# Optimization experiments

Measured on AMD Instinct MI355X. Metric: run time of the kernel, lower is better.

The kernel has to match this reference:

```python
import jax
import jax.numpy as jnp
from jax import lax
import numpy as np

L, B, D_IN, D = 1024, 16, 2048, 2048
K = 3  # n_in == n_out -> k = 3, highway uses x directly


def setup_inputs() -> dict:
    key = jax.random.key(0)
    k1, k2 = jax.random.split(key)
    x = jax.random.normal(k1, (L, B, D_IN), dtype=jnp.float32)
    c0 = jnp.zeros((B, D), dtype=jnp.float32)
    # learned params: projection weight (n_in, n_out*k) and bias (2*n_out)
    weight = jax.random.normal(k2, (D_IN, D * K), dtype=jnp.float32) * (1.0 / np.sqrt(D_IN))
    bias = jnp.zeros((2 * D,), dtype=jnp.float32)
    return {"x": x, "c0": c0, "weight": weight, "bias": bias}


def reference(x, c0, weight, bias):
    # x: [L, B, n_in], c0: [B, d], weight: [n_in, d*3], bias: [2*d]
    Llen, Bsz, _ = x.shape
    d = c0.shape[-1]
    u = jnp.einsum("lbi,ik->lbk", x, weight).reshape(Llen, Bsz, d, K)
    u0 = u[..., 0]                                   # candidate
    g1 = jax.nn.sigmoid(u[..., 1] + bias[:d])        # forget gate
    g2 = jax.nn.sigmoid(u[..., 2] + bias[d:])        # highway/reset gate

    # sequential recurrence: c_t = (c_{t-1} - u0_t) * g1_t + u0_t
    def step(c_prev, inp):
        u0_t, g1_t = inp
        c_t = (c_prev - u0_t) * g1_t + u0_t
        return c_t, c_t

    c_last, cs = lax.scan(step, c0, (u0, g1))
    # h_t = (tanh(c_t) - x_t) * g2_t + x_t   (use_tanh=1, k=3 highway on x)
    h = (jnp.tanh(cs) - x) * g2 + x
    return h, c_last
```

## Files before the change

kernel.cpp:

```cpp
#include <hip/hip_runtime.h>
#include <hip/hip_bf16.h>
#include <cstdint>

#define L_SEQ 1024
#define BSZ   16
#define DIN   2048
#define DD    2048
#define MROWS (L_SEQ * BSZ)
#define NCOLS (3 * DD)
#define BKT   64
#define NT    (DIN / BKT)

typedef __attribute__((ext_vector_type(8))) short  short8;
typedef __attribute__((ext_vector_type(4))) float  f32x4;
typedef __attribute__((ext_vector_type(4))) ushort ushort4v;

typedef const __attribute__((address_space(1))) void* gas_ptr;
typedef __attribute__((address_space(3))) void*       las_ptr;

#define GLOAD16(g, l) __builtin_amdgcn_global_load_lds((gas_ptr)(g), (las_ptr)(l), 16, 0, 0)

__device__ __forceinline__ float bf2f(ushort u) {
    return __uint_as_float(((uint32_t)u) << 16);
}
__device__ __forceinline__ ushort f2bf(float f) {
    uint32_t u = __float_as_uint(f);
    uint32_t r = u + 0x7FFFu + ((u >> 16) & 1u);
    return (ushort)(r >> 16);
}

__global__ __launch_bounds__(256) void pre_kernel(const f32x4* __restrict__ x4,
                                                  ushort4v* __restrict__ xb4,
                                                  const float* __restrict__ W,
                                                  ushort* __restrict__ WT) {
    __shared__ float tile[64][65];
    int bid = blockIdx.x;
    if (bid < 2048) {
        int i = bid * 256 + threadIdx.x;
        const int n4 = MROWS * DIN / 4;
        const int stride = 2048 * 256;
        for (; i < n4; i += stride) {
            f32x4 v = x4[i];
            ushort4v o;
            o.x = f2bf(v.x); o.y = f2bf(v.y); o.z = f2bf(v.z); o.w = f2bf(v.w);
            xb4[i] = o;
        }
    } else {
        int b2 = bid - 2048;
        int k0 = (b2 & 31) * 64;
        int n0 = (b2 >> 5) * 64;
        int c  = threadIdx.x & 63;
        int r0 = threadIdx.x >> 6;
#pragma unroll
        for (int rr = 0; rr < 16; ++rr) {
            int r = r0 + rr * 4;
            tile[r][c] = W[(size_t)(k0 + r) * NCOLS + n0 + c];
        }
        __syncthreads();
#pragma unroll
        for (int rr = 0; rr < 16; ++rr) {
            int r = r0 + rr * 4;
            int n = n0 + r;
            int nprime = (n % 3) * DD + (n / 3);
            WT[(size_t)nprime * DIN + k0 + c] = f2bf(tile[c][r]);
        }
    }
}

#define SLOT(b, s) (&lds8[(((b) << 2) + (s)) * 8192])

#define STAGE_A(b, h, kt) do {                                                   \
    const ushort* _g = Ab + (size_t)((h) * 64 + idx) * DIN + (kt) * BKT + akc;   \
    ushort* _l = SLOT(b, (h)) + tid * 8;                                         \
    GLOAD16(_g, _l);                                                             \
    GLOAD16(_g + (size_t)128 * DIN, _l + 4096);                                  \
} while (0)

#define STAGE_B(b, h2, kt) do {                                                  \
    const ushort* _g0 = Bb + (size_t)(brow0 + (h2) * 32) * DIN + (kt) * BKT + akc;\
    const ushort* _g1 = Bb + (size_t)(brow1 + (h2) * 32) * DIN + (kt) * BKT + akc;\
    ushort* _l = SLOT(b, 2 + (h2)) + tid * 8;                                    \
    GLOAD16(_g0, _l);                                                            \
    GLOAD16(_g1, _l + 4096);                                                     \
} while (0)

#define LD_A2(dst, b, h) do { const ushort* _s = SLOT(b, (h)) + a_rb;            \
    _Pragma("unroll") for (int _m = 0; _m < 4; ++_m) {                           \
        dst[_m][0] = *(const short8*)(_s + _m * 1024 + cs0);                     \
        dst[_m][1] = *(const short8*)(_s + _m * 1024 + cs1); }                   \
} while (0)

#define LD_B(b, h2, bF) do { const ushort* _s = SLOT(b, 2 + (h2)) + b_rb;        \
    _Pragma("unroll") for (int _n = 0; _n < 2; ++_n) {                           \
        bF[_n][0] = *(const short8*)(_s + _n * 1024 + cs0);                      \
        bF[_n][1] = *(const short8*)(_s + _n * 1024 + cs1); }                    \
} while (0)

#define MM(mb, aR, bF, nb) do {                                                  \
    __builtin_amdgcn_s_setprio(1);                                               \
    _Pragma("unroll") for (int _m = 0; _m < 4; ++_m)                             \
    _Pragma("unroll") for (int _n = 0; _n < 2; ++_n) {                           \
        acc[(mb)+_m][(nb)+_n] = __builtin_amdgcn_mfma_f32_16x16x32_bf16(         \
            bF[_n][0], aR[_m][0], acc[(mb)+_m][(nb)+_n], 0, 0, 0);               \
        acc[(mb)+_m][(nb)+_n] = __builtin_amdgcn_mfma_f32_16x16x32_bf16(         \
            bF[_n][1], aR[_m][1], acc[(mb)+_m][(nb)+_n], 0, 0, 0); }             \
    __builtin_amdgcn_s_setprio(0);                                               \
    __builtin_amdgcn_sched_barrier(0);                                           \
} while (0)

#define BARF() do { __builtin_amdgcn_sched_barrier(0);                           \
    __builtin_amdgcn_s_barrier();                                                \
    __builtin_amdgcn_sched_barrier(0); } while (0)

__global__ __launch_bounds__(512, 2) void sru_gemm8(const ushort* __restrict__ A,
                                                    const ushort* __restrict__ Bt,
                                                    const float*  __restrict__ bias,
                                                    ushort* __restrict__ u0,
                                                    ushort* __restrict__ g1,
                                                    ushort* __restrict__ g2) {
    __shared__ alignas(16) ushort lds8[65536];

    int bid = blockIdx.x;
    int swz = (bid & 7) * 192 + (bid >> 3);
    int bm0 = (swz / 24) * 256;
    int bn0 = (swz % 24) * 256;

    int tid  = threadIdx.x;
    int wave = tid >> 6, lane = tid & 63;
    int wm = wave >> 2, wn = wave & 3;

    int idx    = tid >> 3;
    int schunk = (tid & 7) ^ (idx & 7);
    int akc    = schunk * 8;
    int brow0  = (idx >> 5) * 64 + (idx & 31);
    int brow1  = ((idx >> 5) + 2) * 64 + (idx & 31);
    const ushort* Ab = A  + (size_t)bm0 * DIN;
    const ushort* Bb = Bt + (size_t)bn0 * DIN;

    int lrow = lane & 15, lk = lane >> 4, lx = lane & 7;
    int cs0  = ((0 + lk) ^ lx) * 8;
    int cs1  = ((4 + lk) ^ lx) * 8;
    int a_rb = (wm * 64 + lrow) * 64;
    int b_rb = (wn * 32 + lrow) * 64;

    f32x4 acc[8][4];
    f32x4 zero = {0.f, 0.f, 0.f, 0.f};
#pragma unroll
    for (int i = 0; i < 8; ++i)
#pragma unroll
        for (int j = 0; j < 4; ++j) acc[i][j] = zero;

    STAGE_A(0, 0, 0); STAGE_A(0, 1, 0); STAGE_B(0, 0, 0); STAGE_B(0, 1, 0);
    STAGE_A(1, 0, 1); STAGE_B(1, 0, 1);
    asm volatile("s_waitcnt vmcnt(4)" ::: "memory");
    BARF();

    short8 aFA[4][2], aFB[4][2], bF0[2][2], bF1[2][2];
    LD_A2(aFA, 0, 0);
    __builtin_amdgcn_sched_barrier(0);

    for (int t = 0; t < NT; ++t) {
        int cur = t & 1, nxt = cur ^ 1;
        LD_B(cur, 0, bF0);
        LD_B(cur, 1, bF1);
        STAGE_A(nxt, 1, t + 1);
        BARF(); MM(0, aFA, bF0, 0); BARF();
        LD_A2(aFB, cur, 1);
        STAGE_B(nxt, 1, t + 1);
        BARF(); MM(0, aFA, bF1, 2); BARF();
        STAGE_A(cur, 0, t + 2);
        BARF(); MM(4, aFB, bF0, 0); BARF();
        STAGE_B(cur, 0, t + 2);
        asm volatile("s_waitcnt vmcnt(4)" ::: "memory");
        BARF();
        LD_A2(aFA, nxt, 0);
        MM(4, aFB, bF1, 2);
        BARF();
    }
    asm volatile("s_waitcnt vmcnt(0)" ::: "memory");

    int region = bn0 >> 11;
    int colb = (bn0 & (DD - 1)) + wn * 64 + ((lane >> 4) << 2);
    int rowm = bm0 + wm * 128 + (lane & 15);
    if (region == 0) {
#pragma unroll
        for (int j = 0; j < 4; ++j)
#pragma unroll
            for (int i = 0; i < 4; ++i) {
                f32x4 v = acc[i][j];
                uint32_t lo, hi;
                asm("v_cvt_pk_bf16_f32 %0, %1, %2" : "=v"(lo) : "v"(v[0]), "v"(v[1]));
                asm("v_cvt_pk_bf16_f32 %0, %1, %2" : "=v"(hi) : "v"(v[2]), "v"(v[3]));
                uint2 pk; pk.x = lo; pk.y = hi;
                *(uint2*)&u0[(size_t)(rowm + i * 16) * DD + colb + j * 16] = pk;
                f32x4 w = acc[4 + i][j];
                asm("v_cvt_pk_bf16_f32 %0, %1, %2" : "=v"(lo) : "v"(w[0]), "v"(w[1]));
                asm("v_cvt_pk_bf16_f32 %0, %1, %2" : "=v"(hi) : "v"(w[2]), "v"(w[3]));
                pk.x = lo; pk.y = hi;
                *(uint2*)&u0[(size_t)(rowm + 64 + i * 16) * DD + colb + j * 16] = pk;
            }
    } else {
        const float* bp = bias + (size_t)(region - 1) * DD;
        ushort* gp = (region == 1) ? g1 : g2;
#pragma unroll
        for (int j = 0; j < 4; ++j) {
            float4 bv = *(const float4*)&bp[colb + j * 16];
#pragma unroll
            for (int i = 0; i < 8; ++i) {
                f32x4 v = acc[i][j];
                float s0 = 1.f / (1.f + __expf(-(v[0] + bv.x)));
                float s1 = 1.f / (1.f + __expf(-(v[1] + bv.y)));
                float s2 = 1.f / (1.f + __expf(-(v[2] + bv.z)));
                float s3 = 1.f / (1.f + __expf(-(v[3] + bv.w)));
                uint32_t lo, hi;
                asm("v_cvt_pk_bf16_f32 %0, %1, %2" : "=v"(lo) : "v"(s0), "v"(s1));
                asm("v_cvt_pk_bf16_f32 %0, %1, %2" : "=v"(hi) : "v"(s2), "v"(s3));
                uint2 pk; pk.x = lo; pk.y = hi;
                int rr = rowm + (i >> 2) * 64 + (i & 3) * 16;
                *(uint2*)&gp[(size_t)rr * DD + colb + j * 16] = pk;
            }
        }
    }
}

__global__ __launch_bounds__(64) void sru_rec(const ushort* __restrict__ u0,
                                              const ushort* __restrict__ g1,
                                              const ushort* __restrict__ g2,
                                              const ushort* __restrict__ xb,
                                              const float*  __restrict__ c0,
                                              float* __restrict__ h,
                                              float* __restrict__ c_last) {
    int t = blockIdx.x * 64 + threadIdx.x;
    float c = c0[t];
#pragma unroll 16
    for (int l = 0; l < L_SEQ; ++l) {
        int ix = l * (BSZ * DD) + t;
        float uu  = bf2f(u0[ix]);
        float gg1 = bf2f(g1[ix]);
        float gg2 = bf2f(g2[ix]);
        float xx  = bf2f(xb[ix]);
        c = (c - uu) * gg1 + uu;
        float e  = __expf(-2.f * fabsf(c));
        float th = (1.f - e) / (1.f + e);
        th = copysignf(th, c);
        h[ix] = (th - xx) * gg2 + xx;
    }
    c_last[t] = c;
}

extern "C" void kernel_launch(void* const* d_in, const int* in_sizes, int n_in,
                              void* d_out, int out_size, void* d_ws, size_t ws_size,
                              hipStream_t stream) {
    const float* x    = (const float*)d_in[0];
    const float* c0   = (const float*)d_in[1];
    const float* W    = (const float*)d_in[2];
    const float* bias = (const float*)d_in[3];
    float* out = (float*)d_out;

    char* ws = (char*)d_ws;
    ushort* xb = (ushort*)(ws);
    ushort* WT = (ushort*)(ws + 67108864);
    ushort* u0 = (ushort*)(ws + 92274688);
    ushort* g1 = (ushort*)(ws + 159383552);
    ushort* g2 = (ushort*)(ws + 226492416);

    hipLaunchKernelGGL(pre_kernel, dim3(5120), dim3(256), 0, stream,
                       (const f32x4*)x, (ushort4v*)xb, W, WT);
    hipLaunchKernelGGL(sru_gemm8, dim3(1536), dim3(512), 0, stream, xb, WT, bias, u0, g1, g2);
    hipLaunchKernelGGL(sru_rec, dim3(512), dim3(64), 0, stream,
                       u0, g1, g2, xb, c0, out, out + (size_t)MROWS * DD);
}
```

Before: 572.3 us.

## Switch GEMM to 32x32x16 MFMA tiles with new fragment loads and epilogue

Replaces the 16x16x32 bf16 MFMA inner loop with 32x32x16 MFMA, restructuring LDS fragment loads (A loaded per half just before use instead of prefetched) and the accumulator layout to f32x16. Larger MFMA tiles reduce the number of LDS reads and instructions per FLOP. The epilogue is rewritten for the 32x32 output layout. It risks higher register pressure and losing the previous A-fragment prefetch overlap.

```diff
diff --git a/kernel.cpp b/kernel.cpp
--- a/kernel.cpp
+++ b/kernel.cpp
@@ -11,9 +11,10 @@
 #define BKT   64
 #define NT    (DIN / BKT)
 
-typedef __attribute__((ext_vector_type(8))) short  short8;
-typedef __attribute__((ext_vector_type(4))) float  f32x4;
-typedef __attribute__((ext_vector_type(4))) ushort ushort4v;
+typedef __attribute__((ext_vector_type(8)))  short  short8;
+typedef __attribute__((ext_vector_type(4)))  float  f32x4;
+typedef __attribute__((ext_vector_type(16))) float  f32x16;
+typedef __attribute__((ext_vector_type(4)))  ushort ushort4v;
 
 typedef const __attribute__((address_space(1))) void* gas_ptr;
 typedef __attribute__((address_space(3))) void*       las_ptr;
@@ -84,26 +85,23 @@
     GLOAD16(_g1, _l + 4096);                                                     \
 } while (0)
 
-#define LD_A2(dst, b, h) do { const ushort* _s = SLOT(b, (h)) + a_rb;            \
-    _Pragma("unroll") for (int _m = 0; _m < 4; ++_m) {                           \
-        dst[_m][0] = *(const short8*)(_s + _m * 1024 + cs0);                     \
-        dst[_m][1] = *(const short8*)(_s + _m * 1024 + cs1); }                   \
-} while (0)
-
-#define LD_B(b, h2, bF) do { const ushort* _s = SLOT(b, 2 + (h2)) + b_rb;        \
-    _Pragma("unroll") for (int _n = 0; _n < 2; ++_n) {                           \
-        bF[_n][0] = *(const short8*)(_s + _n * 1024 + cs0);                      \
-        bF[_n][1] = *(const short8*)(_s + _n * 1024 + cs1); }                    \
-} while (0)
-
-#define MM(mb, aR, bF, nb) do {                                                  \
+#define LD_A32(dst, b, h) do { const ushort* _s = SLOT(b, (h)) + a_r0;           \
+    _Pragma("unroll") for (int _mf = 0; _mf < 2; ++_mf)                          \
+    _Pragma("unroll") for (int _ks = 0; _ks < 4; ++_ks)                          \
+        dst[_mf * 4 + _ks] = *(const short8*)(_s + _mf * 2048 + ccs[_ks]);       \
+} while (0)
+
+#define LD_B32(dst, b, h2) do { const ushort* _s = SLOT(b, 2 + (h2)) + b_r0;     \
+    _Pragma("unroll") for (int _ks = 0; _ks < 4; ++_ks)                          \
+        dst[_ks] = *(const short8*)(_s + ccs[_ks]);                              \
+} while (0)
+
+#define MM32(mb, bArr, nf, aArr) do {                                            \
     __builtin_amdgcn_s_setprio(1);                                               \
-    _Pragma("unroll") for (int _m = 0; _m < 4; ++_m)                             \
-    _Pragma("unroll") for (int _n = 0; _n < 2; ++_n) {                           \
-        acc[(mb)+_m][(nb)+_n] = __builtin_amdgcn_mfma_f32_16x16x32_bf16(         \
-            bF[_n][0], aR[_m][0], acc[(mb)+_m][(nb)+_n], 0, 0, 0);               \
-        acc[(mb)+_m][(nb)+_n] = __builtin_amdgcn_mfma_f32_16x16x32_bf16(         \
-            bF[_n][1], aR[_m][1], acc[(mb)+_m][(nb)+_n], 0, 0, 0); }             \
+    _Pragma("unroll") for (int _ks = 0; _ks < 4; ++_ks)                          \
+    _Pragma("unroll") for (int _mf = 0; _mf < 2; ++_mf)                          \
+        acc[(mb) + _mf][nf] = __builtin_amdgcn_mfma_f32_32x32x16_bf16(           \
+            bArr[_ks], aArr[_mf * 4 + _ks], acc[(mb) + _mf][nf], 0, 0, 0);       \
     __builtin_amdgcn_s_setprio(0);                                               \
     __builtin_amdgcn_sched_barrier(0);                                           \
 } while (0)
@@ -137,89 +135,89 @@
     const ushort* Ab = A  + (size_t)bm0 * DIN;
     const ushort* Bb = Bt + (size_t)bn0 * DIN;
 
-    int lrow = lane & 15, lk = lane >> 4, lx = lane & 7;
-    int cs0  = ((0 + lk) ^ lx) * 8;
-    int cs1  = ((4 + lk) ^ lx) * 8;
-    int a_rb = (wm * 64 + lrow) * 64;
-    int b_rb = (wn * 32 + lrow) * 64;
-
-    f32x4 acc[8][4];
-    f32x4 zero = {0.f, 0.f, 0.f, 0.f};
-#pragma unroll
-    for (int i = 0; i < 8; ++i)
-#pragma unroll
-        for (int j = 0; j < 4; ++j) acc[i][j] = zero;
+    int l31 = lane & 31, h5 = lane >> 5;
+    int ccs[4];
+#pragma unroll
+    for (int ks = 0; ks < 4; ++ks) ccs[ks] = ((2 * ks + h5) ^ (l31 & 7)) * 8;
+    int a_r0 = (wm * 64 + l31) * 64;
+    int b_r0 = (wn * 32 + l31) * 64;
+
+    f32x16 acc[4][2];
+#pragma unroll
+    for (int i = 0; i < 4; ++i)
+#pragma unroll
+        for (int j = 0; j < 2; ++j)
+#pragma unroll
+            for (int r = 0; r < 16; ++r) acc[i][j][r] = 0.f;
 
     STAGE_A(0, 0, 0); STAGE_A(0, 1, 0); STAGE_B(0, 0, 0); STAGE_B(0, 1, 0);
     STAGE_A(1, 0, 1); STAGE_B(1, 0, 1);
     asm volatile("s_waitcnt vmcnt(4)" ::: "memory");
     BARF();
 
-    short8 aFA[4][2], aFB[4][2], bF0[2][2], bF1[2][2];
-    LD_A2(aFA, 0, 0);
-    __builtin_amdgcn_sched_barrier(0);
+    short8 aLo[8], aHi[8], bF0[4], bF1[4];
 
     for (int t = 0; t < NT; ++t) {
         int cur = t & 1, nxt = cur ^ 1;
-        LD_B(cur, 0, bF0);
-        LD_B(cur, 1, bF1);
+        LD_A32(aLo, cur, 0);
+        LD_B32(bF0, cur, 0);
         STAGE_A(nxt, 1, t + 1);
-        BARF(); MM(0, aFA, bF0, 0); BARF();
-        LD_A2(aFB, cur, 1);
+        BARF(); MM32(0, bF0, 0, aLo); BARF();
+        LD_B32(bF1, cur, 1);
         STAGE_B(nxt, 1, t + 1);
-        BARF(); MM(0, aFA, bF1, 2); BARF();
+        BARF(); MM32(0, bF1, 1, aLo); BARF();
+        LD_A32(aHi, cur, 1);
         STAGE_A(cur, 0, t + 2);
-        BARF(); MM(4, aFB, bF0, 0); BARF();
+        BARF(); MM32(2, bF0, 0, aHi); BARF();
         STAGE_B(cur, 0, t + 2);
         asm volatile("s_waitcnt vmcnt(4)" ::: "memory");
-        BARF();
-        LD_A2(aFA, nxt, 0);
-        MM(4, aFB, bF1, 2);
-        BARF();
+        BARF(); MM32(2, bF1, 1, aHi); BARF();
     }
     asm volatile("s_waitcnt vmcnt(0)" ::: "memory");
 
     int region = bn0 >> 11;
-    int colb = (bn0 & (DD - 1)) + wn * 64 + ((lane >> 4) << 2);
-    int rowm = bm0 + wm * 128 + (lane & 15);
+    int col0 = (bn0 & (DD - 1)) + wn * 64 + 4 * h5;
+    int rowm = bm0 + wm * 128 + l31;
     if (region == 0) {
 #pragma unroll
-        for (int j = 0; j < 4; ++j)
-#pragma unroll
-            for (int i = 0; i < 4; ++i) {
-                f32x4 v = acc[i][j];
-                uint32_t lo, hi;
-                asm("v_cvt_pk_bf16_f32 %0, %1, %2" : "=v"(lo) : "v"(v[0]), "v"(v[1]));
-                asm("v_cvt_pk_bf16_f32 %0, %1, %2" : "=v"(hi) : "v"(v[2]), "v"(v[3]));
-                uint2 pk; pk.x = lo; pk.y = hi;
-                *(uint2*)&u0[(size_t)(rowm + i * 16) * DD + colb + j * 16] = pk;
-                f32x4 w = acc[4 + i][j];
-                asm("v_cvt_pk_bf16_f32 %0, %1, %2" : "=v"(lo) : "v"(w[0]), "v"(w[1]));
-                asm("v_cvt_pk_bf16_f32 %0, %1, %2" : "=v"(hi) : "v"(w[2]), "v"(w[3]));
-                pk.x = lo; pk.y = hi;
-                *(uint2*)&u0[(size_t)(rowm + 64 + i * 16) * DD + colb + j * 16] = pk;
-            }
+        for (int mf = 0; mf < 4; ++mf) {
+            size_t rb = (size_t)(rowm + mf * 32) * DD;
+#pragma unroll
+            for (int nf = 0; nf < 2; ++nf)
+#pragma unroll
+                for (int qb = 0; qb < 4; ++qb) {
+                    uint32_t lo, hi;
+                    float v0 = acc[mf][nf][qb * 4 + 0], v1 = acc[mf][nf][qb * 4 + 1];
+                    float v2 = acc[mf][nf][qb * 4 + 2], v3 = acc[mf][nf][qb * 4 + 3];
+                    asm("v_cvt_pk_bf16_f32 %0, %1, %2" : "=v"(lo) : "v"(v0), "v"(v1));
+                    asm("v_cvt_pk_bf16_f32 %0, %1, %2" : "=v"(hi) : "v"(v2), "v"(v3));
+                    uint2 pk; pk.x = lo; pk.y = hi;
+                    *(uint2*)&u0[rb + col0 + nf * 32 + qb * 8] = pk;
+                }
+        }
     } else {
         const float* bp = bias + (size_t)(region - 1) * DD;
         ushort* gp = (region == 1) ? g1 : g2;
 #pragma unroll
-        for (int j = 0; j < 4; ++j) {
-            float4 bv = *(const float4*)&bp[colb + j * 16];
-#pragma unroll
-            for (int i = 0; i < 8; ++i) {
-                f32x4 v = acc[i][j];
-                float s0 = 1.f / (1.f + __expf(-(v[0] + bv.x)));
-                float s1 = 1.f / (1.f + __expf(-(v[1] + bv.y)));
-                float s2 = 1.f / (1.f + __expf(-(v[2] + bv.z)));
-                float s3 = 1.f / (1.f + __expf(-(v[3] + bv.w)));
-                uint32_t lo, hi;
-                asm("v_cvt_pk_bf16_f32 %0, %1, %2" : "=v"(lo) : "v"(s0), "v"(s1));
-                asm("v_cvt_pk_bf16_f32 %0, %1, %2" : "=v"(hi) : "v"(s2), "v"(s3));
-                uint2 pk; pk.x = lo; pk.y = hi;
-                int rr = rowm + (i >> 2) * 64 + (i & 3) * 16;
-                *(uint2*)&gp[(size_t)rr * DD + colb + j * 16] = pk;
+        for (int nf = 0; nf < 2; ++nf)
+#pragma unroll
+            for (int qb = 0; qb < 4; ++qb) {
+                float4 bv = *(const float4*)&bp[col0 + nf * 32 + qb * 8];
+#pragma unroll
+                for (int mf = 0; mf < 4; ++mf) {
+                    float v0 = acc[mf][nf][qb * 4 + 0], v1 = acc[mf][nf][qb * 4 + 1];
+                    float v2 = acc[mf][nf][qb * 4 + 2], v3 = acc[mf][nf][qb * 4 + 3];
+                    float s0 = 1.f / (1.f + __expf(-(v0 + bv.x)));
+                    float s1 = 1.f / (1.f + __expf(-(v1 + bv.y)));
+                    float s2 = 1.f / (1.f + __expf(-(v2 + bv.z)));
+                    float s3 = 1.f / (1.f + __expf(-(v3 + bv.w)));
+                    uint32_t lo, hi;
+                    asm("v_cvt_pk_bf16_f32 %0, %1, %2" : "=v"(lo) : "v"(s0), "v"(s1));
+                    asm("v_cvt_pk_bf16_f32 %0, %1, %2" : "=v"(hi) : "v"(s2), "v"(s3));
+                    uint2 pk; pk.x = lo; pk.y = hi;
+                    *(uint2*)&gp[(size_t)(rowm + mf * 32) * DD + col0 + nf * 32 + qb * 8] = pk;
+                }
             }
-        }
     }
 }
 
```

Result: slower. 632.7 us (+10.5%).
